# Performance work log

Measured on AMD Instinct MI355X. Metric: run time of the kernel, lower is better.

The kernel has to match this reference:

```python
import jax, jax.numpy as jnp
import numpy as np

B, S, H = 2, 2048, 1024
NH, NKV, HD = 16, 4, 64

def setup_inputs() -> dict:
    key = jax.random.key(0)
    k1, k2, k3, k4, k5 = jax.random.split(key, 5)
    return {
        "hidden_states": jax.random.normal(k1, (B, S, H), dtype=jnp.float32),
        "attention_mask": jnp.ones((B, S), dtype=jnp.int32),
        "wq": jax.random.normal(k2, (H, NH * HD), dtype=jnp.float32) * 0.02,
        "wk": jax.random.normal(k3, (H, NKV * HD), dtype=jnp.float32) * 0.02,
        "wv": jax.random.normal(k4, (H, NKV * HD), dtype=jnp.float32) * 0.02,
        "wo": jax.random.normal(k5, (NH * HD, 1), dtype=jnp.float32) * 0.02,
    }

def reference(hidden_states, attention_mask, wq, wk, wv, wo):
    bsz, seq_len, _ = hidden_states.shape
    n_rep = NH // NKV
    # projections -> (b, h, s, d)
    q = (hidden_states @ wq).reshape(bsz, seq_len, NH, HD).transpose(0, 2, 1, 3)
    k = (hidden_states @ wk).reshape(bsz, seq_len, NKV, HD).transpose(0, 2, 1, 3)
    v = (hidden_states @ wv).reshape(bsz, seq_len, NKV, HD).transpose(0, 2, 1, 3)
    # repeat_kv == repeat_interleave along head axis
    k = jnp.repeat(k, n_rep, axis=1)
    v = jnp.repeat(v, n_rep, axis=1)
    scores = jnp.einsum('bhqd,bhkd->bhqk', q, k) / np.sqrt(HD).astype(np.float32)
    mask = attention_mask[:, None, None, :]  # (b,1,1,k)
    scores = jnp.where(mask == 0, jnp.float32(-jnp.inf), scores)
    attn = jax.nn.softmax(scores, axis=-1)
    out = jnp.einsum('bhqk,bhkd->bqhd', attn, v).reshape(bsz, seq_len, NH * HD)
    return out @ wo  # (b, s, 1)
```

## Files before the change

kernel.cpp:

```cpp
#include <hip/hip_runtime.h>
#include <stdint.h>


typedef __bf16 bf16x8 __attribute__((ext_vector_type(8)));
typedef float f32x4 __attribute__((ext_vector_type(4)));

__device__ inline unsigned short f2bf(float f) {
    unsigned int u = __builtin_bit_cast(unsigned int, f);
    u += 0x7fff + ((u >> 16) & 1);
    return (unsigned short)(u >> 16);
}
__device__ inline bf16x8 ldfrag(const unsigned short* p) {
    uint4 v = *(const uint4*)p;
    return __builtin_bit_cast(bf16x8, v);
}
__device__ inline void gl2lds16(const unsigned short* g, unsigned short* l) {
    __builtin_amdgcn_global_load_lds(
        (const __attribute__((address_space(1))) void*)g,
        (__attribute__((address_space(3))) void*)l, 16, 0, 0);
}

#define SCALE_Q 0.18033688011112042f

__global__ __launch_bounds__(256) void prep_kernel(
    const float* __restrict__ hs, const float* __restrict__ wq,
    const float* __restrict__ wk, const float* __restrict__ wv,
    const float* __restrict__ wo,
    unsigned short* __restrict__ hs_bf, unsigned short* __restrict__ wT)
{
    int bid = blockIdx.x, tid = threadIdx.x;
    if (bid < 4096) {
        int u = bid * 256 + tid;
        float4 v = ((const float4*)hs)[u];
        ushort4 o;
        o.x = f2bf(v.x); o.y = f2bf(v.y); o.z = f2bf(v.z); o.w = f2bf(v.w);
        ((ushort4*)hs_bf)[u] = o;
    } else if (bid < 4416) {
        __shared__ float tile[64 * 65];
        int t = bid - 4096;
        int ntile = t / 16, ctile = t % 16;
        int nb = ntile * 64, cb = ctile * 64;
        int tx = tid & 63, ty = tid >> 6;
        for (int i = 0; i < 16; i++) {
            int cl = i * 4 + ty;
            int n = nb + tx;
            float v = (n < 1024) ? wq[(cb + cl) * 1024 + n] * SCALE_Q
                                 : wk[(cb + cl) * 256 + (n - 1024)];
            tile[cl * 65 + tx] = v;
        }
        __syncthreads();
        for (int i = 0; i < 16; i++) {
            int nl = i * 4 + ty;
            wT[(nb + nl) * 1024 + cb + tx] = f2bf(tile[tx * 65 + nl]);
        }
    } else {
        int u = (bid - 4416) * 256 + tid;
        int n2 = u >> 10, c = u & 1023;
        if (n2 < 16) {
            int h = n2, kv = h >> 2;
            const float* wvr = wv + c * 256 + kv * 64;
            const float* wor = wo + h * 64;
            float s = 0.f;
            #pragma unroll 8
            for (int d = 0; d < 64; d++) s += wvr[d] * wor[d];
            wT[(1280 + n2) * 1024 + c] = f2bf(s);
        } else {
            wT[(1280 + n2) * 1024 + c] = 0;
        }
    }
}

__global__ __launch_bounds__(256) void gemm_kernel(
    const unsigned short* __restrict__ hs_bf, const unsigned short* __restrict__ wT,
    unsigned short* __restrict__ Qp, unsigned short* __restrict__ Kp,
    float* __restrict__ vproj)
{
    __shared__ __align__(16) unsigned short Al[128 * 32];
    __shared__ __align__(16) unsigned short Bl[64 * 32];
    int nt = blockIdx.x, rt = blockIdx.y;
    int tid = threadIdx.x;
    int lane = tid & 63, w = tid >> 6;
    int l15 = lane & 15, quad = lane >> 4;
    int wm = (w >> 1) * 64, wn = (w & 1) * 32;

    f32x4 acc[4][2];
    const f32x4 zero = {0.f, 0.f, 0.f, 0.f};
    for (int i = 0; i < 4; i++) for (int j = 0; j < 2; j++) acc[i][j] = zero;

    int arow = nt * 128, rrow = rt * 64;
    int scol = (lane & 3) * 8;
    const unsigned short* ga = wT + (size_t)(arow + w * 32 + (lane >> 2)) * 1024 + scol;
    const unsigned short* gb = hs_bf + (size_t)(rrow + w * 16 + (lane >> 2)) * 1024 + scol;
    unsigned short* la = Al + (w * 32) * 32;
    unsigned short* lb = Bl + (w * 16) * 32;

    for (int kk = 0; kk < 32; kk++) {
        gl2lds16(ga,             la);
        gl2lds16(ga + 16 * 1024, la + 16 * 32);
        gl2lds16(gb,             lb);
        ga += 32; gb += 32;
        __syncthreads();
        bf16x8 af[4], bfr[2];
        for (int i = 0; i < 4; i++)
            af[i]  = ldfrag(Al + (wm + i * 16 + l15) * 32 + quad * 8);
        for (int j = 0; j < 2; j++)
            bfr[j] = ldfrag(Bl + (wn + j * 16 + l15) * 32 + quad * 8);
        for (int i = 0; i < 4; i++)
            for (int j = 0; j < 2; j++)
                acc[i][j] = __builtin_amdgcn_mfma_f32_16x16x32_bf16(af[i], bfr[j], acc[i][j], 0, 0, 0);
        __syncthreads();
    }

    for (int i = 0; i < 4; i++) {
        for (int j = 0; j < 2; j++) {
            int nw = nt * 128 + wm + i * 16 + quad * 4;
            int r  = rt * 64 + wn + j * 16 + l15;
            if (nt < 8) {
                ushort4 o;
                o.x = f2bf(acc[i][j][0]); o.y = f2bf(acc[i][j][1]);
                o.z = f2bf(acc[i][j][2]); o.w = f2bf(acc[i][j][3]);
                *(ushort4*)(Qp + (size_t)r * 1024 + nw) = o;
            } else if (nt < 10) {
                ushort4 o;
                o.x = f2bf(acc[i][j][0]); o.y = f2bf(acc[i][j][1]);
                o.z = f2bf(acc[i][j][2]); o.w = f2bf(acc[i][j][3]);
                *(ushort4*)(Kp + (size_t)r * 256 + (nw - 1024)) = o;
            } else {
                for (int rg = 0; rg < 4; rg++) {
                    int h = nw + rg - 1280;
                    if (h < 16)
                        vproj[((size_t)(r >> 11) * 16 + h) * 2048 + (r & 2047)] = acc[i][j][rg];
                }
            }
        }
    }
}

__global__ __launch_bounds__(256) void attn_kernel(
    const unsigned short* __restrict__ Qp, const unsigned short* __restrict__ Kp,
    const float* __restrict__ vproj, const int* __restrict__ mask,
    float2* __restrict__ part)
{
    __shared__ __align__(16) unsigned short Kl[256 * 80];
    __shared__ __align__(16) float vpml[4 * 256];
    __shared__ __align__(16) float biasl[256];
    int qt = blockIdx.x;
    int b = blockIdx.y >> 2, kv = blockIdx.y & 3;
    int ks = blockIdx.z;
    int tid = threadIdx.x, lane = tid & 63, w = tid >> 6;
    int l15 = lane & 15, quad = lane >> 4;
    int h = kv * 4 + w;
    int qrow0 = qt * 64;

    bf16x8 qf[4][2];
    for (int qs = 0; qs < 4; qs++) {
        const unsigned short* qp =
            Qp + (size_t)(b * 2048 + qrow0 + qs * 16 + l15) * 1024 + h * 64 + quad * 8;
        qf[qs][0] = ldfrag(qp);
        qf[qs][1] = ldfrag(qp + 32);
    }

    float num[4] = {0.f, 0.f, 0.f, 0.f}, den[4] = {0.f, 0.f, 0.f, 0.f};
    for (int kt = 0; kt < 2; kt++) {
        int k0 = ks * 512 + kt * 256;
        for (int it = 0; it < 8; it++) {
            int u = it * 256 + tid;
            int row = u >> 3, ch = u & 7;
            *(uint4*)(Kl + row * 80 + ch * 8) =
                *(const uint4*)(Kp + (size_t)(b * 2048 + k0 + row) * 256 + kv * 64 + ch * 8);
        }
        {
            int h2 = tid >> 6, kk = (tid & 63) * 4;
            *(float4*)(vpml + h2 * 256 + kk) =
                *(const float4*)(vproj + ((size_t)b * 16 + kv * 4 + h2) * 2048 + k0 + kk);
        }
        if (tid < 64) {
            int4 mm = *(const int4*)(mask + b * 2048 + k0 + tid * 4);
            float4 bb;
            bb.x = mm.x ? 0.f : -30000.f;
            bb.y = mm.y ? 0.f : -30000.f;
            bb.z = mm.z ? 0.f : -30000.f;
            bb.w = mm.w ? 0.f : -30000.f;
            *(float4*)(biasl + tid * 4) = bb;
        }
        __syncthreads();

        for (int t8 = 0; t8 < 16; t8++) {
            const unsigned short* kb = Kl + (t8 * 16 + l15) * 80 + quad * 8;
            bf16x8 a0 = ldfrag(kb);
            bf16x8 a1 = ldfrag(kb + 32);
            f32x4 vpm4 = *(const f32x4*)(vpml + w * 256 + t8 * 16 + quad * 4);
            f32x4 c4   = *(const f32x4*)(biasl + t8 * 16 + quad * 4);
            for (int qs = 0; qs < 4; qs++) {
                f32x4 d = __builtin_amdgcn_mfma_f32_16x16x32_bf16(a0, qf[qs][0], c4, 0, 0, 0);
                d = __builtin_amdgcn_mfma_f32_16x16x32_bf16(a1, qf[qs][1], d, 0, 0, 0);
                for (int r = 0; r < 4; r++) {
                    float e = __builtin_amdgcn_exp2f(d[r]);
                    num[qs] += e * vpm4[r];
                    den[qs] += e;
                }
            }
        }
        __syncthreads();
    }
    for (int qs = 0; qs < 4; qs++) {
        float n = num[qs], dd = den[qs];
        n += __shfl_xor(n, 16);  n += __shfl_xor(n, 32);
        dd += __shfl_xor(dd, 16); dd += __shfl_xor(dd, 32);
        if (quad == 0) {
            int q = qrow0 + qs * 16 + l15;
            part[((size_t)(b * 2048 + q) * 16 + h) * 4 + ks] = make_float2(n, dd);
        }
    }
}

__global__ __launch_bounds__(256) void combine_kernel(
    const float2* __restrict__ part, float* __restrict__ out)
{
    int wid = (blockIdx.x * 256 + threadIdx.x) >> 6;
    int lane = threadIdx.x & 63;
    const float2* base = part + (size_t)wid * 64;
    float2 p = base[lane];
    p.x += __shfl_xor(p.x, 1); p.y += __shfl_xor(p.y, 1);
    p.x += __shfl_xor(p.x, 2); p.y += __shfl_xor(p.y, 2);
    float v = p.x / p.y;
    for (int m = 4; m <= 32; m <<= 1) v += __shfl_xor(v, m);
    if (lane == 0) out[wid] = v;
}

extern "C" void kernel_launch(void* const* d_in, const int* in_sizes, int n_in,
                              void* d_out, int out_size, void* d_ws, size_t ws_size,
                              hipStream_t stream)
{
    const float* hs  = (const float*)d_in[0];
    const int* mask  = (const int*)d_in[1];
    const float* wq  = (const float*)d_in[2];
    const float* wk  = (const float*)d_in[3];
    const float* wv  = (const float*)d_in[4];
    const float* wo  = (const float*)d_in[5];

    char* ws = (char*)d_ws;
    unsigned short* hs_bf = (unsigned short*)ws;
    unsigned short* wT    = (unsigned short*)(ws + 8388608);
    unsigned short* Qp    = (unsigned short*)(ws + 11272192);
    unsigned short* Kp    = (unsigned short*)(ws + 19660800);
    float* vproj          = (float*)(ws + 21757952);
    float2* part          = (float2*)(ws + 22020096);

    prep_kernel<<<4928, 256, 0, stream>>>(hs, wq, wk, wv, wo, hs_bf, wT);
    gemm_kernel<<<dim3(11, 64), 256, 0, stream>>>(hs_bf, wT, Qp, Kp, vproj);
    attn_kernel<<<dim3(32, 8, 4), 256, 0, stream>>>(Qp, Kp, vproj, mask, part);
    combine_kernel<<<1024, 256, 0, stream>>>(part, (float*)d_out);
}
```

Measured before the change: 161.4 us.

## Load K, V-proj and mask bias directly from global in attention, drop LDS staging

The attention kernel no longer stages K tiles, projected V values and the mask bias through shared memory with block-wide barriers. Each wave now reads its MFMA fragments directly from global memory (relying on L1/L2 for reuse across the four heads of a KV group). The mask-to-bias conversion moves into the prep kernel, and launch bounds request higher occupancy. This removes LDS traffic and synchronisation but repeats global/cache reads four times per block and gives up explicit reuse.

```diff
diff --git a/kernel.cpp b/kernel.cpp
--- a/kernel.cpp
+++ b/kernel.cpp
@@ -25,8 +25,9 @@
 __global__ __launch_bounds__(256) void prep_kernel(
     const float* __restrict__ hs, const float* __restrict__ wq,
     const float* __restrict__ wk, const float* __restrict__ wv,
-    const float* __restrict__ wo,
-    unsigned short* __restrict__ hs_bf, unsigned short* __restrict__ wT)
+    const float* __restrict__ wo, const int* __restrict__ mask,
+    unsigned short* __restrict__ hs_bf, unsigned short* __restrict__ wT,
+    float* __restrict__ biasf)
 {
     int bid = blockIdx.x, tid = threadIdx.x;
     if (bid < 4096) {
@@ -53,7 +54,7 @@
             int nl = i * 4 + ty;
             wT[(nb + nl) * 1024 + cb + tx] = f2bf(tile[tx * 65 + nl]);
         }
-    } else {
+    } else if (bid < 4928) {
         int u = (bid - 4416) * 256 + tid;
         int n2 = u >> 10, c = u & 1023;
         if (n2 < 16) {
@@ -67,6 +68,9 @@
         } else {
             wT[(1280 + n2) * 1024 + c] = 0;
         }
+    } else {
+        int u = (bid - 4928) * 256 + tid;
+        biasf[u] = mask[u] ? 0.f : -30000.f;
     }
 }
 
@@ -136,14 +140,11 @@
     }
 }
 
-__global__ __launch_bounds__(256) void attn_kernel(
+__global__ __launch_bounds__(256, 4) void attn_kernel(
     const unsigned short* __restrict__ Qp, const unsigned short* __restrict__ Kp,
-    const float* __restrict__ vproj, const int* __restrict__ mask,
+    const float* __restrict__ vproj, const float* __restrict__ biasf,
     float2* __restrict__ part)
 {
-    __shared__ __align__(16) unsigned short Kl[256 * 80];
-    __shared__ __align__(16) float vpml[4 * 256];
-    __shared__ __align__(16) float biasl[256];
     int qt = blockIdx.x;
     int b = blockIdx.y >> 2, kv = blockIdx.y & 3;
     int ks = blockIdx.z;
@@ -160,48 +161,28 @@
         qf[qs][1] = ldfrag(qp + 32);
     }
 
+    const unsigned short* kp =
+        Kp + (size_t)(b * 2048 + ks * 512 + l15) * 256 + kv * 64 + quad * 8;
+    const float* vp = vproj + ((size_t)b * 16 + h) * 2048 + ks * 512 + quad * 4;
+    const float* bp = biasf + b * 2048 + ks * 512 + quad * 4;
+
     float num[4] = {0.f, 0.f, 0.f, 0.f}, den[4] = {0.f, 0.f, 0.f, 0.f};
-    for (int kt = 0; kt < 2; kt++) {
-        int k0 = ks * 512 + kt * 256;
-        for (int it = 0; it < 8; it++) {
-            int u = it * 256 + tid;
-            int row = u >> 3, ch = u & 7;
-            *(uint4*)(Kl + row * 80 + ch * 8) =
-                *(const uint4*)(Kp + (size_t)(b * 2048 + k0 + row) * 256 + kv * 64 + ch * 8);
-        }
-        {
-            int h2 = tid >> 6, kk = (tid & 63) * 4;
-            *(float4*)(vpml + h2 * 256 + kk) =
-                *(const float4*)(vproj + ((size_t)b * 16 + kv * 4 + h2) * 2048 + k0 + kk);
-        }
-        if (tid < 64) {
-            int4 mm = *(const int4*)(mask + b * 2048 + k0 + tid * 4);
-            float4 bb;
-            bb.x = mm.x ? 0.f : -30000.f;
-            bb.y = mm.y ? 0.f : -30000.f;
-            bb.z = mm.z ? 0.f : -30000.f;
-            bb.w = mm.w ? 0.f : -30000.f;
-            *(float4*)(biasl + tid * 4) = bb;
-        }
-        __syncthreads();
-
-        for (int t8 = 0; t8 < 16; t8++) {
-            const unsigned short* kb = Kl + (t8 * 16 + l15) * 80 + quad * 8;
-            bf16x8 a0 = ldfrag(kb);
-            bf16x8 a1 = ldfrag(kb + 32);
-            f32x4 vpm4 = *(const f32x4*)(vpml + w * 256 + t8 * 16 + quad * 4);
-            f32x4 c4   = *(const f32x4*)(biasl + t8 * 16 + quad * 4);
-            for (int qs = 0; qs < 4; qs++) {
-                f32x4 d = __builtin_amdgcn_mfma_f32_16x16x32_bf16(a0, qf[qs][0], c4, 0, 0, 0);
-                d = __builtin_amdgcn_mfma_f32_16x16x32_bf16(a1, qf[qs][1], d, 0, 0, 0);
-                for (int r = 0; r < 4; r++) {
-                    float e = __builtin_amdgcn_exp2f(d[r]);
-                    num[qs] += e * vpm4[r];
-                    den[qs] += e;
-                }
+    #pragma unroll 2
+    for (int t8 = 0; t8 < 32; t8++) {
+        bf16x8 a0 = ldfrag(kp);
+        bf16x8 a1 = ldfrag(kp + 32);
+        f32x4 vpm4 = *(const f32x4*)vp;
+        f32x4 c4   = *(const f32x4*)bp;
+        kp += 16 * 256; vp += 16; bp += 16;
+        for (int qs = 0; qs < 4; qs++) {
+            f32x4 d = __builtin_amdgcn_mfma_f32_16x16x32_bf16(a0, qf[qs][0], c4, 0, 0, 0);
+            d = __builtin_amdgcn_mfma_f32_16x16x32_bf16(a1, qf[qs][1], d, 0, 0, 0);
+            for (int r = 0; r < 4; r++) {
+                float e = __builtin_amdgcn_exp2f(d[r]);
+                num[qs] += e * vpm4[r];
+                den[qs] += e;
             }
         }
-        __syncthreads();
     }
     for (int qs = 0; qs < 4; qs++) {
         float n = num[qs], dd = den[qs];
@@ -246,9 +227,10 @@
     unsigned short* Kp    = (unsigned short*)(ws + 19660800);
     float* vproj          = (float*)(ws + 21757952);
     float2* part          = (float2*)(ws + 22020096);
-
-    prep_kernel<<<4928, 256, 0, stream>>>(hs, wq, wk, wv, wo, hs_bf, wT);
+    float* biasf          = (float*)(ws + 24117248);
+
+    prep_kernel<<<4944, 256, 0, stream>>>(hs, wq, wk, wv, wo, mask, hs_bf, wT, biasf);
     gemm_kernel<<<dim3(11, 64), 256, 0, stream>>>(hs_bf, wT, Qp, Kp, vproj);
-    attn_kernel<<<dim3(32, 8, 4), 256, 0, stream>>>(Qp, Kp, vproj, mask, part);
+    attn_kernel<<<dim3(32, 8, 4), 256, 0, stream>>>(Qp, Kp, vproj, biasf, part);
     combine_kernel<<<1024, 256, 0, stream>>>(part, (float*)d_out);
 }
```

Measured after the change: 153.6 us. 4.9% less time.
